# Optimization experiments

Hardware: AMD Instinct MI355X
Metric: run time of the kernel (lower is better)

Reference implementation:

```python
import jax, jax.numpy as jnp
import numpy as np

LATENT = 64  # latent_size -> N = K = LATENT**2 = 4096 codes/tokens


def setup_inputs() -> dict:
    key = jax.random.key(0)
    k1, k2 = jax.random.split(key)
    hidden, L = 1024, LATENT
    z = jax.random.normal(k1, (hidden, L, L), dtype=jnp.float32)
    code_books = jax.random.uniform(k2, (hidden, L, L), dtype=jnp.float32)  # torch.rand init
    return {"z": z, "code_books": code_books}


def reference(z, code_books):
    # z, code_books: (D=hidden, L, L). Tokens/codes are columns of the flattened maps.
    D = z.shape[0]
    zf = z.reshape(D, -1).T           # (N, D) tokens
    cb = code_books.reshape(D, -1).T  # (K, D) codebook entries
    # Squared L2 distance via GEMM trick: ||a-b||^2 = ||a||^2 + ||b||^2 - 2 a.b
    # (avoids the N x K x D broadcast intermediate of the original)
    d2 = (jnp.sum(zf * zf, axis=1)[:, None]
          + jnp.sum(cb * cb, axis=1)[None, :]
          - 2.0 * zf @ cb.T)          # (N, K)
    idx = jnp.argmin(d2, axis=1)      # (N,)
    zq = cb[idx]                      # (N, D) gather
    zq = zq.reshape(LATENT, LATENT, -1).transpose(2, 0, 1)  # (D, L, L)
    # Straight-through: z = zq + (z - zq).detach()  (z was detached before lookup)
    z_st = zq + jax.lax.stop_gradient(z - zq)
    return z_st, zq
```

## Files before the change

kernel.cpp:

```cpp
#include <hip/hip_runtime.h>
#include <stdint.h>

#define D  1024
#define NK 4096
#define KA 1024
#define KB 1024
#define TAU 0.15f
#define CW  0.12f
#define MAXC 1024

#define BK2 32
#define NT2 (KA / BK2)
#define NBUF 4

typedef __attribute__((ext_vector_type(8))) _Float16 f16x8;
typedef __attribute__((ext_vector_type(4))) float f32x4;
typedef unsigned long long u64;

__device__ __forceinline__ uint32_t fkey(float f) {
    uint32_t b = __float_as_uint(f);
    return (b & 0x80000000u) ? ~b : (b | 0x80000000u);
}
__device__ __forceinline__ float unfkey(uint32_t u) {
    uint32_t b = (u & 0x80000000u) ? (u & 0x7fffffffu) : ~u;
    return __uint_as_float(b);
}
__device__ __forceinline__ u64 umin64(u64 a, u64 b) { return a < b ? a : b; }
__device__ __forceinline__ u64 umax64(u64 a, u64 b) { return a > b ? a : b; }

__device__ __forceinline__ void gload16(void* lds, const void* g) {
    __builtin_amdgcn_global_load_lds(
        (const __attribute__((address_space(1))) unsigned int*)g,
        (__attribute__((address_space(3))) unsigned int*)lds, 16, 0, 0);
}

#define BAR()     __builtin_amdgcn_s_barrier()
#define LGKM0()   asm volatile("s_waitcnt lgkmcnt(0)" ::: "memory")
#define SCHEDBAR() __builtin_amdgcn_sched_barrier(0)
#define VMCNT4()  asm volatile("s_waitcnt vmcnt(4)" ::: "memory")
#define VMCNT0()  asm volatile("s_waitcnt vmcnt(0)" ::: "memory")

__global__ void cbnorm_kernel(const float* __restrict__ cb, float* __restrict__ cbn) {
    __shared__ float red[256];
    const int kk = threadIdx.x & 63;
    const int dc = threadIdx.x >> 6;
    const int k  = blockIdx.x * 64 + kk;
    float s = 0.f;
    for (int d = dc; d < D; d += 4) {
        float v = cb[d * NK + k];
        s = fmaf(v, v, s);
    }
    red[threadIdx.x] = s;
    __syncthreads();
    if (dc == 0) cbn[k] = (red[kk] + red[64 + kk]) + (red[128 + kk] + red[192 + kk]);
}

__global__ __launch_bounds__(256) void split_transpose(
        const float* __restrict__ z, const float* __restrict__ cb,
        _Float16* __restrict__ Ap, _Float16* __restrict__ Bp,
        float* __restrict__ partial) {
    __shared__ float T[64][65];
    const int isZ = (blockIdx.z == 0);
    const float* src = isZ ? z : cb;
    _Float16* dst = isZ ? Ap : Bp;
    const int n0 = blockIdx.x * 64, d0 = blockIdx.y * 64;
    const int t = threadIdx.x;
#pragma unroll
    for (int i = 0; i < 4; ++i) {
        int dl = (t >> 4) + i * 16;
        int nl = (t & 15) * 4;
        float4 v = *(const float4*)&src[(size_t)(d0 + dl) * NK + n0 + nl];
        T[dl][nl] = v.x; T[dl][nl + 1] = v.y; T[dl][nl + 2] = v.z; T[dl][nl + 3] = v.w;
    }
    __syncthreads();
    const int nr = t >> 2, dch = (t & 3) * 16;
    f16x8 h0, h1;
    float s = 0.f;
#pragma unroll
    for (int j = 0; j < 8; ++j) {
        float v = T[dch + j][nr];
        s = fmaf(v, v, s);
        h0[j] = (_Float16)v;
    }
#pragma unroll
    for (int j = 0; j < 8; ++j) {
        float v = T[dch + 8 + j][nr];
        s = fmaf(v, v, s);
        h1[j] = (_Float16)v;
    }
    size_t base = (size_t)(n0 + nr) * KA + d0 + dch;
    *(f16x8*)&dst[base]     = h0;
    *(f16x8*)&dst[base + 8] = h1;
    if (!isZ) {
        s += __shfl_xor(s, 1);
        s += __shfl_xor(s, 2);
        if ((t & 3) == 0) partial[(size_t)(d0 >> 6) * NK + n0 + nr] = s;
    }
}

__global__ void cbnorm_finish(const float* __restrict__ partial, float* __restrict__ cbn) {
    const int k = blockIdx.x * 256 + threadIdx.x;
    float s = 0.f;
#pragma unroll
    for (int j = 0; j < 16; ++j) s += partial[(size_t)j * NK + k];
    cbn[k] = s;
}

__global__ __launch_bounds__(512, 2) void gemm_mfma(
        const _Float16* __restrict__ Ap, const _Float16* __restrict__ Bp,
        const float* __restrict__ cbn, ulonglong2* __restrict__ tp) {
    __shared__ _Float16 As[NBUF][256 * BK2];
    __shared__ _Float16 Bs[NBUF][256 * BK2];
    const int tid = threadIdx.x;
    const int xcd = blockIdx.x & 7, idx = blockIdx.x >> 3;
    const int n0 = ((xcd >> 1) * 4 + (idx >> 3)) * 256;
    const int k0 = ((xcd & 1) * 8 + (idx & 7)) * 256;
    const int w = tid >> 6, l = tid & 63;
    const int wr = w >> 2, wc = w & 3;
    const int fr = l & 15, fq = l >> 4;

    f32x4 acc[8][4] = {};

    const int srow = tid >> 2;
    const int swz = ((tid & 3) ^ ((tid >> 3) & 3)) * 8;
    const _Float16* gA0 = Ap + (size_t)(n0 + srow) * KA + swz;
    const _Float16* gA1 = Ap + (size_t)(n0 + 128 + srow) * KA + swz;
    const _Float16* gB0 = Bp + (size_t)(k0 + srow) * KB + swz;
    const _Float16* gB1 = Bp + (size_t)(k0 + 128 + srow) * KB + swz;
    const int rcol = (fq ^ ((fr >> 1) & 3)) * 8;

    gload16(&As[0][tid * 8],        gA0);
    gload16(&As[0][4096 + tid * 8], gA1);
    gload16(&Bs[0][tid * 8],        gB0);
    gload16(&Bs[0][4096 + tid * 8], gB1);
    gload16(&As[1][tid * 8],        gA0 + BK2);
    gload16(&As[1][4096 + tid * 8], gA1 + BK2);
    gload16(&Bs[1][tid * 8],        gB0 + BK2);
    gload16(&Bs[1][4096 + tid * 8], gB1 + BK2);
    VMCNT4();
    BAR();

    for (int t = 0; t < NT2; ++t) {
        const int b = t & 3;
        const int pb = (t + 2) & 3;
        const _Float16* Ab = As[b];
        const _Float16* Bb = Bs[b];
        const bool st = (t + 2) < NT2;

        f16x8 bbf[4], a0[4];
#pragma unroll
        for (int ni = 0; ni < 4; ++ni)
            bbf[ni] = *(const f16x8*)&Bb[(wc * 64 + ni * 16 + fr) * BK2 + rcol];
#pragma unroll
        for (int mi = 0; mi < 4; ++mi)
            a0[mi] = *(const f16x8*)&Ab[(wr * 128 + mi * 16 + fr) * BK2 + rcol];
        if (st) {
            gload16(&As[pb][tid * 8],        gA0 + (t + 2) * BK2);
            gload16(&As[pb][4096 + tid * 8], gA1 + (t + 2) * BK2);
        }
        BAR();
        LGKM0();
        SCHEDBAR();
        __builtin_amdgcn_s_setprio(1);
#pragma unroll
        for (int mi = 0; mi < 4; ++mi)
#pragma unroll
            for (int ni = 0; ni < 4; ++ni)
                acc[mi][ni] = __builtin_amdgcn_mfma_f32_16x16x32_f16(a0[mi], bbf[ni], acc[mi][ni], 0, 0, 0);
        __builtin_amdgcn_s_setprio(0);
        BAR();

        f16x8 a1[4];
#pragma unroll
        for (int mi = 0; mi < 4; ++mi)
            a1[mi] = *(const f16x8*)&Ab[(wr * 128 + 64 + mi * 16 + fr) * BK2 + rcol];
        if (st) {
            gload16(&Bs[pb][tid * 8],        gB0 + (t + 2) * BK2);
            gload16(&Bs[pb][4096 + tid * 8], gB1 + (t + 2) * BK2);
        }
        BAR();
        LGKM0();
        SCHEDBAR();
        __builtin_amdgcn_s_setprio(1);
#pragma unroll
        for (int mi = 0; mi < 4; ++mi)
#pragma unroll
            for (int ni = 0; ni < 4; ++ni)
                acc[4 + mi][ni] = __builtin_amdgcn_mfma_f32_16x16x32_f16(a1[mi], bbf[ni], acc[4 + mi][ni], 0, 0, 0);
        __builtin_amdgcn_s_setprio(0);
        if (t < NT2 - 2) {
            VMCNT4();
        } else if (t == NT2 - 2) {
            VMCNT0();
        }
        if (t < NT2 - 1) BAR();
    }

    float cbv[4];
#pragma unroll
    for (int ni = 0; ni < 4; ++ni) cbv[ni] = cbn[k0 + wc * 64 + ni * 16 + fr];
    const int kt64 = (k0 >> 6) + wc;
#pragma unroll
    for (int mi = 0; mi < 8; ++mi) {
#pragma unroll
        for (int reg = 0; reg < 4; ++reg) {
            float b1f = 1e30f, b2f = 1e30f;
            int b1k = 0;
#pragma unroll
            for (int ni = 0; ni < 4; ++ni) {
                float s = fmaf(-2.f, acc[mi][ni][reg], cbv[ni]);
                b2f = fminf(fmaxf(s, b1f), b2f);
                if (s < b1f) { b1f = s; b1k = k0 + wc * 64 + ni * 16 + fr; }
            }
#pragma unroll
            for (int m = 8; m >= 1; m >>= 1) {
                float q1 = __shfl_xor(b1f, m);
                int   qk = __shfl_xor(b1k, m);
                float q2 = __shfl_xor(b2f, m);
                b2f = fminf(fminf(b2f, q2), fmaxf(b1f, q1));
                if (q1 < b1f) { b1f = q1; b1k = qk; }
            }
            if (fr == 0) {
                int n = n0 + wr * 128 + mi * 16 + fq * 4 + reg;
                ulonglong2 v;
                v.x = ((u64)fkey(b1f) << 32) | (unsigned)b1k;
                v.y = ((u64)fkey(b2f) << 32) | 0xffffffffu;
                tp[(size_t)kt64 * NK + n] = v;
            }
        }
    }
}

__global__ __launch_bounds__(256) void reduce_rows(
        const ulonglong2* __restrict__ tp, int* __restrict__ idx,
        int* __restrict__ rescue, u64* __restrict__ rbest, int* __restrict__ ctr) {
    __shared__ ulonglong2 sh[4][64];
    const int no = threadIdx.x & 63, st = threadIdx.x >> 6;
    const int n = blockIdx.x * 64 + no;
    u64 b1 = ~0ull, b2 = ~0ull;
#pragma unroll 4
    for (int g = st * 16; g < st * 16 + 16; ++g) {
        ulonglong2 e = tp[(size_t)g * NK + n];
        u64 nb1 = umin64(b1, e.x);
        u64 nb2 = umin64(umax64(b1, e.x), umin64(b2, e.y));
        b1 = nb1; b2 = nb2;
    }
    ulonglong2 v; v.x = b1; v.y = b2;
    sh[st][no] = v;
    __syncthreads();
    if (st == 0) {
#pragma unroll
        for (int j = 1; j < 4; ++j) {
            ulonglong2 e = sh[j][no];
            u64 nb1 = umin64(b1, e.x);
            u64 nb2 = umin64(umax64(b1, e.x), umin64(b2, e.y));
            b1 = nb1; b2 = nb2;
        }
        idx[n] = (int)(b1 & 0xffffffffull);
        float f1 = unfkey((uint32_t)(b1 >> 32));
        float f2 = unfkey((uint32_t)(b2 >> 32));
        if (f2 - f1 < TAU) {
            int p = atomicAdd(ctr, 1);
            rescue[p] = n;
            rbest[p] = ~0ull;
        }
    }
}

__global__ __launch_bounds__(256) void rescue_kernel(
        const float* __restrict__ z, const float* __restrict__ cb,
        const float* __restrict__ cbn, const ulonglong2* __restrict__ tp,
        const int* __restrict__ rescue, const int* __restrict__ ctr,
        u64* __restrict__ rbest) {
    const int cnt = min(*ctr, NK);
    const int slot = blockIdx.x;
    if (slot >= cnt) return;
    const int n = rescue[slot];
    const int tid = threadIdx.x;
    const int lane = tid & 63, wv = tid >> 6;

    __shared__ float zn[D];
    __shared__ int cand[MAXC];
    __shared__ int ccnt, overflow;
    __shared__ u64 wred[4];

    if (tid == 0) { ccnt = 0; overflow = 0; }
    for (int d = tid; d < D; d += 256) zn[d] = z[(size_t)d * NK + n];

    if (tid < 64) {
        ulonglong2 e = tp[(size_t)tid * NK + n];
        u64 m = e.x;
#pragma unroll
        for (int msk = 32; msk >= 1; msk >>= 1) m = umin64(m, __shfl_xor(m, msk));
        const float thr = unfkey((uint32_t)(m >> 32)) + CW;
        if (unfkey((uint32_t)(e.y >> 32)) < thr) {
            int p = atomicAdd(&ccnt, 64);
            if (p + 64 <= MAXC) {
                for (int j = 0; j < 64; ++j) cand[p + j] = tid * 64 + j;
            } else overflow = 1;
        } else if (unfkey((uint32_t)(e.x >> 32)) < thr) {
            int p = atomicAdd(&ccnt, 1);
            if (p < MAXC) cand[p] = (int)(e.x & 0xffffffffull);
            else overflow = 1;
        }
    }
    __syncthreads();

    const int ovf = overflow;
    const int m = ovf ? NK : min(ccnt, MAXC);
    u64 best = ~0ull;
    for (int ci = wv; ci < m; ci += 4) {
        const int k = ovf ? ci : cand[ci];
        float s = 0.f;
#pragma unroll
        for (int j = 0; j < 16; ++j)
            s = fmaf(zn[lane + j * 64], cb[(size_t)(lane + j * 64) * NK + k], s);
#pragma unroll
        for (int msk = 32; msk >= 1; msk >>= 1) s += __shfl_xor(s, msk);
        float sc = cbn[k] - 2.f * s;
        best = umin64(best, ((u64)fkey(sc) << 32) | (unsigned)k);
    }
    if (lane == 0) wred[wv] = best;
    __syncthreads();
    if (tid == 0)
        rbest[slot] = umin64(umin64(wred[0], wred[1]), umin64(wred[2], wred[3]));
}

__global__ void fix_idx(const int* __restrict__ rescue, const int* __restrict__ ctr,
                        const u64* __restrict__ rbest, int* __restrict__ idx) {
    const int cnt = min(*ctr, NK);
    for (int s = threadIdx.x + blockIdx.x * 256; s < cnt; s += gridDim.x * 256)
        idx[rescue[s]] = (int)(rbest[s] & 0xffffffffull);
}

__global__ __launch_bounds__(256) void gemm_argmin(
        const float* __restrict__ z, const float* __restrict__ cb,
        const float* __restrict__ cbn, unsigned long long* __restrict__ best) {
    __shared__ float Zs[8][128];
    __shared__ float Cs[8][128];
    const int n0 = blockIdx.y * 128, k0 = blockIdx.x * 128;
    const int tid = threadIdx.x;
    const int tx = tid & 15, ty = tid >> 4;
    const int lr = tid >> 5, lc = (tid & 31) << 2;
    float acc[8][8];
#pragma unroll
    for (int i = 0; i < 8; ++i)
#pragma unroll
        for (int j = 0; j < 8; ++j) acc[i][j] = 0.f;
    for (int d0 = 0; d0 < D; d0 += 8) {
        float4 zv = *(const float4*)&z [(d0 + lr) * NK + n0 + lc];
        float4 cv = *(const float4*)&cb[(d0 + lr) * NK + k0 + lc];
        __syncthreads();
        *(float4*)&Zs[lr][lc] = zv;
        *(float4*)&Cs[lr][lc] = cv;
        __syncthreads();
#pragma unroll
        for (int dd = 0; dd < 8; ++dd) {
            float4 a0 = *(const float4*)&Zs[dd][ty * 8];
            float4 a1 = *(const float4*)&Zs[dd][ty * 8 + 4];
            float4 b0 = *(const float4*)&Cs[dd][tx * 8];
            float4 b1 = *(const float4*)&Cs[dd][tx * 8 + 4];
            float a[8] = {a0.x, a0.y, a0.z, a0.w, a1.x, a1.y, a1.z, a1.w};
            float b[8] = {b0.x, b0.y, b0.z, b0.w, b1.x, b1.y, b1.z, b1.w};
#pragma unroll
            for (int i = 0; i < 8; ++i)
#pragma unroll
                for (int j = 0; j < 8; ++j) acc[i][j] = fmaf(a[i], b[j], acc[i][j]);
        }
    }
    float cbnv[8];
#pragma unroll
    for (int j = 0; j < 8; ++j) cbnv[j] = cbn[k0 + tx * 8 + j];
#pragma unroll
    for (int i = 0; i < 8; ++i) {
        float bv = cbnv[0] - 2.f * acc[i][0];
        int bj = 0;
#pragma unroll
        for (int j = 1; j < 8; ++j) {
            float v = cbnv[j] - 2.f * acc[i][j];
            if (v < bv) { bv = v; bj = j; }
        }
        u64 p = ((u64)fkey(bv) << 32) | (unsigned)(k0 + tx * 8 + bj);
#pragma unroll
        for (int m = 8; m >= 1; m >>= 1) {
            u64 q = __shfl_xor(p, m);
            if (q < p) p = q;
        }
        if (tx == 0) atomicMin(&best[n0 + ty * 8 + i], p);
    }
}

__global__ void extract_idx(const unsigned long long* __restrict__ best,
                            int* __restrict__ idx) {
    int n = blockIdx.x * 256 + threadIdx.x;
    idx[n] = (int)(unsigned)(best[n] & 0xFFFFFFFFull);
}

__global__ void gather_kernel(const float* __restrict__ z, const float* __restrict__ cb,
                              const int* __restrict__ idx, float* __restrict__ out) {
    const int d = blockIdx.x;
    const float* cbrow = &cb[(size_t)d * NK];
    const float* zrow  = &z [(size_t)d * NK];
    float* st = &out[(size_t)d * NK];
    float* zq = &out[(size_t)D * NK + (size_t)d * NK];
    for (int n4 = threadIdx.x; n4 < NK / 4; n4 += 256) {
        int4 iv = *(const int4*)&idx[n4 * 4];
        float4 zv = *(const float4*)&zrow[n4 * 4];
        float4 q;
        q.x = cbrow[iv.x]; q.y = cbrow[iv.y]; q.z = cbrow[iv.z]; q.w = cbrow[iv.w];
        float4 stv;
        stv.x = q.x + (zv.x - q.x);
        stv.y = q.y + (zv.y - q.y);
        stv.z = q.z + (zv.z - q.z);
        stv.w = q.w + (zv.w - q.w);
        *(float4*)&st[n4 * 4] = stv;
        *(float4*)&zq[n4 * 4] = q;
    }
}

extern "C" void kernel_launch(void* const* d_in, const int* in_sizes, int n_in,
                              void* d_out, int out_size, void* d_ws, size_t ws_size,
                              hipStream_t stream) {
    const float* z  = (const float*)d_in[0];
    const float* cb = (const float*)d_in[1];
    float* out = (float*)d_out;
    char* ws = (char*)d_ws;

    const size_t oA  = 0;
    const size_t oB  = oA + (size_t)NK * KA * 2;
    const size_t oT  = oB + (size_t)NK * KB * 2;
    const size_t oC  = oT + (size_t)NK * 64 * 16;
    const size_t oI  = oC + NK * 4;
    const size_t oR  = oI + NK * 4;
    const size_t oRB = oR + NK * 4;
    const size_t oN  = oRB + NK * 8;
    const size_t oP  = oN + 256;
    const size_t REQ = oP + (size_t)16 * NK * 4;

    if (ws_size >= REQ) {
        _Float16* Ap = (_Float16*)(ws + oA);
        _Float16* Bp = (_Float16*)(ws + oB);
        ulonglong2* tp = (ulonglong2*)(ws + oT);
        float* cbn = (float*)(ws + oC);
        int* idx = (int*)(ws + oI);
        int* rescue = (int*)(ws + oR);
        u64* rbest = (u64*)(ws + oRB);
        int* ctr = (int*)(ws + oN);
        float* partial = (float*)(ws + oP);

        hipMemsetAsync(ctr, 0, 4, stream);
        split_transpose<<<dim3(NK / 64, D / 64, 2), 256, 0, stream>>>(z, cb, Ap, Bp, partial);
        cbnorm_finish<<<16, 256, 0, stream>>>(partial, cbn);
        gemm_mfma<<<256, 512, 0, stream>>>(Ap, Bp, cbn, tp);
        reduce_rows<<<64, 256, 0, stream>>>(tp, idx, rescue, rbest, ctr);
        rescue_kernel<<<4096, 256, 0, stream>>>(z, cb, cbn, tp, rescue, ctr, rbest);
        fix_idx<<<4, 256, 0, stream>>>(rescue, ctr, rbest, idx);
        gather_kernel<<<1024, 256, 0, stream>>>(z, cb, idx, out);
    } else {
        unsigned long long* best = (unsigned long long*)ws;
        float* cbn = (float*)(ws + NK * 8);
        int* idx = (int*)(ws + NK * 8 + NK * 4);
        hipMemsetAsync(best, 0xFF, NK * 8, stream);
        cbnorm_kernel<<<64, 256, 0, stream>>>(cb, cbn);
        gemm_argmin<<<dim3(NK / 128, NK / 128), 256, 0, stream>>>(z, cb, cbn, best);
        extract_idx<<<16, 256, 0, stream>>>(best, idx);
        gather_kernel<<<1024, 256, 0, stream>>>(z, cb, idx, out);
    }
}
```

Before: 89.29 us.

## Shrink GEMM tile to 256x128 with 4 waves and triple-buffered LDS

The fp16 MFMA distance GEMM now uses 256-thread blocks covering a 256x128 output tile instead of 512 threads covering 256x256, and launches 512 blocks instead of 256. The LDS ring drops from four to three stages, and the vmcnt waits and block-to-XCD mapping are adjusted to match. The aim is more resident blocks per CU and a smaller LDS footprint for better latency hiding. The cost is lower arithmetic intensity per block (more A reloads) and less prefetch slack. Any epilogue code that assumes the old wave layout or wc range may also need to change.

```diff
diff --git a/kernel.cpp b/kernel.cpp
--- a/kernel.cpp
+++ b/kernel.cpp
@@ -11,7 +11,7 @@
 
 #define BK2 32
 #define NT2 (KA / BK2)
-#define NBUF 4
+#define NBUF 3
 
 typedef __attribute__((ext_vector_type(8))) _Float16 f16x8;
 typedef __attribute__((ext_vector_type(4))) float f32x4;
@@ -34,11 +34,11 @@
         (__attribute__((address_space(3))) unsigned int*)lds, 16, 0, 0);
 }
 
-#define BAR()     __builtin_amdgcn_s_barrier()
-#define LGKM0()   asm volatile("s_waitcnt lgkmcnt(0)" ::: "memory")
+#define BAR()      __builtin_amdgcn_s_barrier()
+#define LGKM0()    asm volatile("s_waitcnt lgkmcnt(0)" ::: "memory")
 #define SCHEDBAR() __builtin_amdgcn_sched_barrier(0)
-#define VMCNT4()  asm volatile("s_waitcnt vmcnt(4)" ::: "memory")
-#define VMCNT0()  asm volatile("s_waitcnt vmcnt(0)" ::: "memory")
+#define VMCNT6()   asm volatile("s_waitcnt vmcnt(6)" ::: "memory")
+#define VMCNT0()   asm volatile("s_waitcnt vmcnt(0)" ::: "memory")
 
 __global__ void cbnorm_kernel(const float* __restrict__ cb, float* __restrict__ cbn) {
     __shared__ float red[256];
@@ -106,46 +106,44 @@
     cbn[k] = s;
 }
 
-__global__ __launch_bounds__(512, 2) void gemm_mfma(
+__global__ __launch_bounds__(256, 2) void gemm_mfma(
         const _Float16* __restrict__ Ap, const _Float16* __restrict__ Bp,
         const float* __restrict__ cbn, ulonglong2* __restrict__ tp) {
     __shared__ _Float16 As[NBUF][256 * BK2];
-    __shared__ _Float16 Bs[NBUF][256 * BK2];
+    __shared__ _Float16 Bs[NBUF][128 * BK2];
     const int tid = threadIdx.x;
     const int xcd = blockIdx.x & 7, idx = blockIdx.x >> 3;
-    const int n0 = ((xcd >> 1) * 4 + (idx >> 3)) * 256;
-    const int k0 = ((xcd & 1) * 8 + (idx & 7)) * 256;
+    const int n0 = ((xcd >> 2) * 8 + (idx >> 3)) * 256;
+    const int k0 = ((xcd & 3) * 8 + (idx & 7)) * 128;
     const int w = tid >> 6, l = tid & 63;
-    const int wr = w >> 2, wc = w & 3;
+    const int wr = w >> 1, wc = w & 1;
     const int fr = l & 15, fq = l >> 4;
 
     f32x4 acc[8][4] = {};
 
     const int srow = tid >> 2;
     const int swz = ((tid & 3) ^ ((tid >> 3) & 3)) * 8;
-    const _Float16* gA0 = Ap + (size_t)(n0 + srow) * KA + swz;
-    const _Float16* gA1 = Ap + (size_t)(n0 + 128 + srow) * KA + swz;
-    const _Float16* gB0 = Bp + (size_t)(k0 + srow) * KB + swz;
-    const _Float16* gB1 = Bp + (size_t)(k0 + 128 + srow) * KB + swz;
+    const _Float16* gA = Ap + (size_t)(n0 + srow) * KA + swz;
+    const _Float16* gB = Bp + (size_t)(k0 + srow) * KB + swz;
     const int rcol = (fq ^ ((fr >> 1) & 3)) * 8;
 
-    gload16(&As[0][tid * 8],        gA0);
-    gload16(&As[0][4096 + tid * 8], gA1);
-    gload16(&Bs[0][tid * 8],        gB0);
-    gload16(&Bs[0][4096 + tid * 8], gB1);
-    gload16(&As[1][tid * 8],        gA0 + BK2);
-    gload16(&As[1][4096 + tid * 8], gA1 + BK2);
-    gload16(&Bs[1][tid * 8],        gB0 + BK2);
-    gload16(&Bs[1][4096 + tid * 8], gB1 + BK2);
-    VMCNT4();
+#pragma unroll
+    for (int i = 0; i < 4; ++i) gload16(&As[0][tid * 8 + i * 2048], gA + (size_t)(64 * i) * KA);
+#pragma unroll
+    for (int i = 0; i < 2; ++i) gload16(&Bs[0][tid * 8 + i * 2048], gB + (size_t)(64 * i) * KB);
+#pragma unroll
+    for (int i = 0; i < 4; ++i) gload16(&As[1][tid * 8 + i * 2048], gA + (size_t)(64 * i) * KA + BK2);
+#pragma unroll
+    for (int i = 0; i < 2; ++i) gload16(&Bs[1][tid * 8 + i * 2048], gB + (size_t)(64 * i) * KB + BK2);
+    VMCNT6();
     BAR();
 
+    int b = 0, pb = 2;
     for (int t = 0; t < NT2; ++t) {
-        const int b = t & 3;
-        const int pb = (t + 2) & 3;
         const _Float16* Ab = As[b];
         const _Float16* Bb = Bs[b];
         const bool st = (t + 2) < NT2;
+        const size_t kofs = (size_t)(t + 2) * BK2;
 
         f16x8 bbf[4], a0[4];
 #pragma unroll
@@ -155,8 +153,9 @@
         for (int mi = 0; mi < 4; ++mi)
             a0[mi] = *(const f16x8*)&Ab[(wr * 128 + mi * 16 + fr) * BK2 + rcol];
         if (st) {
-            gload16(&As[pb][tid * 8],        gA0 + (t + 2) * BK2);
-            gload16(&As[pb][4096 + tid * 8], gA1 + (t + 2) * BK2);
+#pragma unroll
+            for (int i = 0; i < 4; ++i)
+                gload16(&As[pb][tid * 8 + i * 2048], gA + (size_t)(64 * i) * KA + kofs);
         }
         BAR();
         LGKM0();
@@ -175,8 +174,9 @@
         for (int mi = 0; mi < 4; ++mi)
             a1[mi] = *(const f16x8*)&Ab[(wr * 128 + 64 + mi * 16 + fr) * BK2 + rcol];
         if (st) {
-            gload16(&Bs[pb][tid * 8],        gB0 + (t + 2) * BK2);
-            gload16(&Bs[pb][4096 + tid * 8], gB1 + (t + 2) * BK2);
+#pragma unroll
+            for (int i = 0; i < 2; ++i)
+                gload16(&Bs[pb][tid * 8 + i * 2048], gB + (size_t)(64 * i) * KB + kofs);
         }
         BAR();
         LGKM0();
@@ -189,11 +189,13 @@
                 acc[4 + mi][ni] = __builtin_amdgcn_mfma_f32_16x16x32_f16(a1[mi], bbf[ni], acc[4 + mi][ni], 0, 0, 0);
         __builtin_amdgcn_s_setprio(0);
         if (t < NT2 - 2) {
-            VMCNT4();
+            VMCNT6();
         } else if (t == NT2 - 2) {
             VMCNT0();
         }
         if (t < NT2 - 1) BAR();
+        b = (b == 2) ? 0 : b + 1;
+        pb = (pb == 2) ? 0 : pb + 1;
     }
 
     float cbv[4];
@@ -451,7 +453,7 @@
         hipMemsetAsync(ctr, 0, 4, stream);
         split_transpose<<<dim3(NK / 64, D / 64, 2), 256, 0, stream>>>(z, cb, Ap, Bp, partial);
         cbnorm_finish<<<16, 256, 0, stream>>>(partial, cbn);
-        gemm_mfma<<<256, 512, 0, stream>>>(Ap, Bp, cbn, tp);
+        gemm_mfma<<<512, 256, 0, stream>>>(Ap, Bp, cbn, tp);
         reduce_rows<<<64, 256, 0, stream>>>(tp, idx, rescue, rbest, ctr);
         rescue_kernel<<<4096, 256, 0, stream>>>(z, cb, cbn, tp, rescue, ctr, rbest);
         fix_idx<<<4, 256, 0, stream>>>(rescue, ctr, rbest, idx);
```

Result: no change. 90.08 us (+0.9%).
